# Performance work log

Hardware: AMD Instinct MI355X
Metric: run time of the kernel (lower is better)

Reference implementation:

```python
import jax, jax.numpy as jnp
import numpy as np

N_TOTAL = 524288  # total entity embeddings in flat ragged buffer
A = 262144        # number of actors
D = 256           # d_model
C = 32            # n_choice


def setup_inputs() -> dict:
    key = jax.random.key(0)
    k1, k2, k3, k4, k5 = jax.random.split(key, 5)
    x_data = jax.random.normal(k1, (N_TOTAL, D), dtype=jnp.float32)
    W = jax.random.normal(k2, (C, D), dtype=jnp.float32) * 0.01  # layer_init std=0.01
    b = jnp.zeros((C,), dtype=jnp.float32)
    actors = jax.random.randint(k3, (A,), 0, N_TOTAL, dtype=jnp.int64)
    mask = jax.random.randint(k4, (A, C), 0, 2, dtype=jnp.int32)
    mask = mask.at[:, 0].set(1)  # guarantee at least one valid choice per actor
    pa = jax.random.randint(k5, (A,), 0, C, dtype=jnp.int64)
    # prev_actions must be valid under the mask (as a real rollout would be)
    valid = jnp.take_along_axis(mask, pa[:, None], axis=1).squeeze(-1)
    prev_actions = jnp.where(valid != 0, pa, 0)
    return {"x_data": x_data, "W": W, "b": b, "actors": actors,
            "mask": mask, "prev_actions": prev_actions}


def reference(x_data, W, b, actors, mask, prev_actions):
    # gather actor embeddings: [A, D]
    actor_embeds = x_data[actors]
    # linear projection: [A, C]
    logits = jnp.einsum('ad,cd->ac', actor_embeds, W) + b
    # masked fill with -inf where mask == 0
    logits = jnp.where(mask == 0, -jnp.inf, logits)
    # Categorical: normalized logits = log_softmax
    logp = jax.nn.log_softmax(logits, axis=-1)
    p = jnp.exp(logp)
    action = prev_actions  # prev_actions provided -> no sampling
    logprob = jnp.take_along_axis(logp, action[:, None], axis=1).squeeze(-1)
    # entropy: -sum p*logp over valid entries (0*(-inf) -> 0)
    entropy = -jnp.sum(jnp.where(mask != 0, p * logp, 0.0), axis=-1)
    return action, logprob, entropy, logp
```

## Files before the change

### kernel.cpp

```cpp
#include <hip/hip_runtime.h>
#include <math.h>


constexpr int A_TOTAL = 262144;
constexpr int DMODEL  = 256;
constexpr int NCHOICE = 32;
constexpr int APB     = 64;
constexpr int PADC    = 36;

#define MASK_NEG 1.0e30f

#define DPP_SUM_STEP(x, ctrl)                                              \
    (x) += __int_as_float(__builtin_amdgcn_update_dpp(                     \
        0, __float_as_int(x), (ctrl), 0xf, 0xf, true))
#define DPP_MAX_STEP(x, ctrl)                                              \
    (x) = fmaxf((x), __int_as_float(__builtin_amdgcn_update_dpp(           \
        0, __float_as_int(x), (ctrl), 0xf, 0xf, true)))

#define DPP_REDUCE_DG(x)                                                   \
    do { DPP_SUM_STEP(x, 0xB1); DPP_SUM_STEP(x, 0x4E);                     \
         DPP_SUM_STEP(x, 0x128); DPP_SUM_STEP(x, 0x124); } while (0)
#define DPP_RED8_SUM(x)                                                    \
    do { DPP_SUM_STEP(x, 0xB1); DPP_SUM_STEP(x, 0x4E);                     \
         DPP_SUM_STEP(x, 0x141); } while (0)
#define DPP_RED8_MAX(x)                                                    \
    do { DPP_MAX_STEP(x, 0xB1); DPP_MAX_STEP(x, 0x4E);                     \
         DPP_MAX_STEP(x, 0x141); } while (0)

__global__ __launch_bounds__(256, 2)
void cat_action_head(const float* __restrict__ x_data,
                     const float* __restrict__ W,
                     const float* __restrict__ bvec,
                     const int*   __restrict__ actors,
                     const int*   __restrict__ mask,
                     const int*   __restrict__ prev_actions,
                     float* __restrict__ out)
{
    const int t  = threadIdx.x;
    const int wv = t >> 6;
    const int ln = t & 63;
    const int dg = ln & 15;
    const int cg = ln >> 4;

    float* out_action  = out;
    float* out_logprob = out + A_TOTAL;
    float* out_entropy = out + 2 * A_TOTAL;
    float* out_logp    = out + 3 * A_TOTAL;

    __shared__ float xs[4][2][8][DMODEL];
    __shared__ float part[APB][PADC];

    const int bbase = blockIdx.x * APB;
    const int wb    = bbase + wv * 16;

    const int q  = ln & 7;
    const int p0 = wv * 16 + (ln >> 3);
    const int p1 = p0 + 8;
    const int a0 = bbase + p0;
    const int a1 = bbase + p1;
    const int4   mv0 = *reinterpret_cast<const int4*>(&mask[(size_t)a0 * NCHOICE + q * 4]);
    const int4   mv1 = *reinterpret_cast<const int4*>(&mask[(size_t)a1 * NCHOICE + q * 4]);
    const float4 bq  = *reinterpret_cast<const float4*>(&bvec[q * 4]);
    const int    act0 = prev_actions[a0];
    const int    act1 = prev_actions[a1];

    int acts[16];
    {
        const int4 v0 = *reinterpret_cast<const int4*>(&actors[wb]);
        const int4 v1 = *reinterpret_cast<const int4*>(&actors[wb + 4]);
        const int4 v2 = *reinterpret_cast<const int4*>(&actors[wb + 8]);
        const int4 v3 = *reinterpret_cast<const int4*>(&actors[wb + 12]);
        acts[0]=v0.x; acts[1]=v0.y; acts[2]=v0.z; acts[3]=v0.w;
        acts[4]=v1.x; acts[5]=v1.y; acts[6]=v1.z; acts[7]=v1.w;
        acts[8]=v2.x; acts[9]=v2.y; acts[10]=v2.z; acts[11]=v2.w;
        acts[12]=v3.x; acts[13]=v3.y; acts[14]=v3.z; acts[15]=v3.w;
    }

#define STAGE(BUF, C)                                                       \
    do {                                                                    \
        _Pragma("unroll")                                                   \
        for (int j = 0; j < 8; ++j) {                                       \
            const float* src = x_data + (size_t)acts[(C) * 8 + j] * DMODEL  \
                             + ln * 4;                                      \
            __builtin_amdgcn_global_load_lds(                               \
                (const __attribute__((address_space(1))) void*)src,         \
                (__attribute__((address_space(3))) void*)&xs[wv][BUF][j][0],\
                16, 0, 0);                                                  \
        }                                                                   \
    } while (0)

    STAGE(0, 0);

    float4 Wf[8][4];
#pragma unroll
    for (int k = 0; k < 8; ++k) {
        const float* Wr = W + (size_t)(cg * 8 + k) * DMODEL + dg * 4;
#pragma unroll
        for (int j = 0; j < 4; ++j)
            Wf[k][j] = *reinterpret_cast<const float4*>(Wr + j * 64);
    }

    STAGE(1, 1);

#define LDR(DST, BUF, II)                                                   \
    do {                                                                    \
        const float* xrow_ = &xs[wv][BUF][II][dg * 4];                      \
        _Pragma("unroll")                                                   \
        for (int j = 0; j < 4; ++j)                                         \
            DST[j] = *reinterpret_cast<const float4*>(xrow_ + j * 64);      \
    } while (0)

#define COMPUTE(XV, C, II)                                                  \
    do {                                                                    \
        float acc[8] = {0.f,0.f,0.f,0.f,0.f,0.f,0.f,0.f};                   \
        _Pragma("unroll")                                                   \
        for (int j = 0; j < 4; ++j) {                                       \
            _Pragma("unroll")                                               \
            for (int k = 0; k < 8; ++k) {                                   \
                acc[k] = fmaf(XV[j].x, Wf[k][j].x, acc[k]);                 \
                acc[k] = fmaf(XV[j].y, Wf[k][j].y, acc[k]);                 \
                acc[k] = fmaf(XV[j].z, Wf[k][j].z, acc[k]);                 \
                acc[k] = fmaf(XV[j].w, Wf[k][j].w, acc[k]);                 \
            }                                                               \
        }                                                                   \
        _Pragma("unroll")                                                   \
        for (int k = 0; k < 8; ++k) DPP_REDUCE_DG(acc[k]);                  \
        if (dg == 0) {                                                      \
            const int p_ = wv * 16 + (C) * 8 + (II);                        \
            float4 v0_; v0_.x=acc[0]; v0_.y=acc[1]; v0_.z=acc[2]; v0_.w=acc[3]; \
            float4 v1_; v1_.x=acc[4]; v1_.y=acc[5]; v1_.z=acc[6]; v1_.w=acc[7]; \
            *reinterpret_cast<float4*>(&part[p_][cg * 8])     = v0_;        \
            *reinterpret_cast<float4*>(&part[p_][cg * 8 + 4]) = v1_;        \
        }                                                                   \
    } while (0)

#define GEMV_CHUNK(C)                                                       \
    do {                                                                    \
        float4 xva[4], xvb[4];                                              \
        LDR(xva, (C) & 1, 0);                                               \
        _Pragma("unroll")                                                   \
        for (int ii = 0; ii < 8; ii += 2) {                                 \
            if (ii + 1 < 8) LDR(xvb, (C) & 1, ii + 1);                      \
            COMPUTE(xva, C, ii);                                            \
            if (ii + 2 < 8) LDR(xva, (C) & 1, ii + 2);                      \
            COMPUTE(xvb, C, ii + 1);                                        \
        }                                                                   \
    } while (0)

    asm volatile("s_waitcnt vmcnt(8)" ::: "memory");
    GEMV_CHUNK(0);
    asm volatile("s_waitcnt vmcnt(0)" ::: "memory");
    GEMV_CHUNK(1);

#define EPILOGUE(PROW, AEP, MV, ACT)                                        \
    do {                                                                    \
        const float4 pv = *reinterpret_cast<const float4*>(&part[PROW][q * 4]); \
        const float lg0 = (MV).x ? pv.x + bq.x : -MASK_NEG;                 \
        const float lg1 = (MV).y ? pv.y + bq.y : -MASK_NEG;                 \
        const float lg2 = (MV).z ? pv.z + bq.z : -MASK_NEG;                 \
        const float lg3 = (MV).w ? pv.w + bq.w : -MASK_NEG;                 \
        float mx = fmaxf(fmaxf(lg0, lg1), fmaxf(lg2, lg3));                 \
        DPP_RED8_MAX(mx);                                                   \
        const float e0 = expf(lg0 - mx);                                    \
        const float e1 = expf(lg1 - mx);                                    \
        const float e2 = expf(lg2 - mx);                                    \
        const float e3 = expf(lg3 - mx);                                    \
        float se = (e0 + e1) + (e2 + e3);                                   \
        DPP_RED8_SUM(se);                                                   \
        const float lse = mx + logf(se);                                    \
        const float rse = 1.0f / se;                                        \
        const float lp0 = lg0 - lse;                                        \
        const float lp1 = lg1 - lse;                                        \
        const float lp2 = lg2 - lse;                                        \
        const float lp3 = lg3 - lse;                                        \
        float4 lpv; lpv.x=lp0; lpv.y=lp1; lpv.z=lp2; lpv.w=lp3;             \
        *reinterpret_cast<float4*>(                                         \
            &out_logp[(size_t)(AEP) * NCHOICE + q * 4]) = lpv;              \
        float ent = fmaf(e0, lp0, fmaf(e1, lp1, fmaf(e2, lp2, e3 * lp3)));  \
        DPP_RED8_SUM(ent);                                                  \
        float sel = ((ACT) == q * 4 + 0) ? lp0 : 0.0f;                      \
        sel = ((ACT) == q * 4 + 1) ? lp1 : sel;                             \
        sel = ((ACT) == q * 4 + 2) ? lp2 : sel;                             \
        sel = ((ACT) == q * 4 + 3) ? lp3 : sel;                             \
        DPP_RED8_SUM(sel);                                                  \
        if (q == 0) {                                                       \
            out_logprob[AEP] = sel;                                         \
            out_entropy[AEP] = -ent * rse;                                  \
            out_action[AEP]  = (float)(ACT);                                \
        }                                                                   \
    } while (0)

    EPILOGUE(p0, a0, mv0, act0);
    EPILOGUE(p1, a1, mv1, act1);

#undef EPILOGUE
#undef GEMV_CHUNK
#undef COMPUTE
#undef LDR
#undef STAGE
}

extern "C" void kernel_launch(void* const* d_in, const int* in_sizes, int n_in,
                              void* d_out, int out_size, void* d_ws, size_t ws_size,
                              hipStream_t stream)
{
    const float* x_data = (const float*)d_in[0];
    const float* W      = (const float*)d_in[1];
    const float* bvec   = (const float*)d_in[2];
    const int*   actors = (const int*)d_in[3];
    const int*   mask   = (const int*)d_in[4];
    const int*   prev   = (const int*)d_in[5];
    float*       o      = (float*)d_out;

    const int nblocks = A_TOTAL / APB;
    cat_action_head<<<nblocks, 256, 0, stream>>>(x_data, W, bvec, actors, mask,
                                                 prev, o);
}
```

Measured before the change: 94.75 us.

## Make each wave loop over 128 actors with double-buffered gathers

Each wave now processes 128 actors in 16 chunks of 8 instead of 16 actors, keeping W in registers across all chunks. This cuts the per-wave reloading of the 32 KB weight matrix and shrinks the grid from 4096 to 512 blocks. Gathers of the next chunk's embeddings go into LDS through global_load_lds while the current chunk is computed, and the actor indices, masks and previous actions are prefetched two chunks ahead. The pipeline depends on hand-tuned vmcnt wait counts, and a single wave of blocks gives less parallelism to hide latency with.

Result: slower. 97.29 us (+2.7%).

```diff
diff --git a/kernel.cpp b/kernel.cpp
--- a/kernel.cpp
+++ b/kernel.cpp
@@ -5,8 +5,9 @@
 constexpr int A_TOTAL = 262144;
 constexpr int DMODEL  = 256;
 constexpr int NCHOICE = 32;
-constexpr int APB     = 64;
 constexpr int PADC    = 36;
+constexpr int APW     = 128;
+constexpr int APB     = 512;
 
 #define MASK_NEG 1.0e30f
 
@@ -41,6 +42,8 @@
     const int ln = t & 63;
     const int dg = ln & 15;
     const int cg = ln >> 4;
+    const int q  = ln & 7;
+    const int ar = ln >> 3;
 
     float* out_action  = out;
     float* out_logprob = out + A_TOTAL;
@@ -48,117 +51,66 @@
     float* out_logp    = out + 3 * A_TOTAL;
 
     __shared__ float xs[4][2][8][DMODEL];
-    __shared__ float part[APB][PADC];
-
-    const int bbase = blockIdx.x * APB;
-    const int wb    = bbase + wv * 16;
-
-    const int q  = ln & 7;
-    const int p0 = wv * 16 + (ln >> 3);
-    const int p1 = p0 + 8;
-    const int a0 = bbase + p0;
-    const int a1 = bbase + p1;
-    const int4   mv0 = *reinterpret_cast<const int4*>(&mask[(size_t)a0 * NCHOICE + q * 4]);
-    const int4   mv1 = *reinterpret_cast<const int4*>(&mask[(size_t)a1 * NCHOICE + q * 4]);
-    const float4 bq  = *reinterpret_cast<const float4*>(&bvec[q * 4]);
-    const int    act0 = prev_actions[a0];
-    const int    act1 = prev_actions[a1];
-
-    int acts[16];
-    {
-        const int4 v0 = *reinterpret_cast<const int4*>(&actors[wb]);
-        const int4 v1 = *reinterpret_cast<const int4*>(&actors[wb + 4]);
-        const int4 v2 = *reinterpret_cast<const int4*>(&actors[wb + 8]);
-        const int4 v3 = *reinterpret_cast<const int4*>(&actors[wb + 12]);
-        acts[0]=v0.x; acts[1]=v0.y; acts[2]=v0.z; acts[3]=v0.w;
-        acts[4]=v1.x; acts[5]=v1.y; acts[6]=v1.z; acts[7]=v1.w;
-        acts[8]=v2.x; acts[9]=v2.y; acts[10]=v2.z; acts[11]=v2.w;
-        acts[12]=v3.x; acts[13]=v3.y; acts[14]=v3.z; acts[15]=v3.w;
-    }
-
-#define STAGE(BUF, C)                                                       \
-    do {                                                                    \
+    __shared__ float part[4][8][PADC];
+
+    const int wbase = (blockIdx.x * 4 + wv) * APW;
+
+#define STAGE(P, A0, A1)                                                    \
+    do {                                                                    \
+        const int av_[8] = {(A0).x,(A0).y,(A0).z,(A0).w,                    \
+                            (A1).x,(A1).y,(A1).z,(A1).w};                   \
         _Pragma("unroll")                                                   \
         for (int j = 0; j < 8; ++j) {                                       \
-            const float* src = x_data + (size_t)acts[(C) * 8 + j] * DMODEL  \
-                             + ln * 4;                                      \
+            const float* src_ = x_data + (size_t)av_[j] * DMODEL + ln * 4;  \
             __builtin_amdgcn_global_load_lds(                               \
-                (const __attribute__((address_space(1))) void*)src,         \
-                (__attribute__((address_space(3))) void*)&xs[wv][BUF][j][0],\
+                (const __attribute__((address_space(1))) void*)src_,        \
+                (__attribute__((address_space(3))) void*)&xs[wv][P][j][0],  \
                 16, 0, 0);                                                  \
         }                                                                   \
     } while (0)
 
-    STAGE(0, 0);
-
-    float4 Wf[8][4];
-#pragma unroll
-    for (int k = 0; k < 8; ++k) {
-        const float* Wr = W + (size_t)(cg * 8 + k) * DMODEL + dg * 4;
-#pragma unroll
-        for (int j = 0; j < 4; ++j)
-            Wf[k][j] = *reinterpret_cast<const float4*>(Wr + j * 64);
-    }
-
-    STAGE(1, 1);
-
-#define LDR(DST, BUF, II)                                                   \
-    do {                                                                    \
-        const float* xrow_ = &xs[wv][BUF][II][dg * 4];                      \
+#define GEMV(P)                                                             \
+    do {                                                                    \
         _Pragma("unroll")                                                   \
-        for (int j = 0; j < 4; ++j)                                         \
-            DST[j] = *reinterpret_cast<const float4*>(xrow_ + j * 64);      \
-    } while (0)
-
-#define COMPUTE(XV, C, II)                                                  \
-    do {                                                                    \
-        float acc[8] = {0.f,0.f,0.f,0.f,0.f,0.f,0.f,0.f};                   \
-        _Pragma("unroll")                                                   \
-        for (int j = 0; j < 4; ++j) {                                       \
+        for (int ii = 0; ii < 8; ++ii) {                                    \
+            const float* xrow_ = &xs[wv][P][ii][dg * 4];                    \
+            float4 xv_[4];                                                  \
             _Pragma("unroll")                                               \
-            for (int k = 0; k < 8; ++k) {                                   \
-                acc[k] = fmaf(XV[j].x, Wf[k][j].x, acc[k]);                 \
-                acc[k] = fmaf(XV[j].y, Wf[k][j].y, acc[k]);                 \
-                acc[k] = fmaf(XV[j].z, Wf[k][j].z, acc[k]);                 \
-                acc[k] = fmaf(XV[j].w, Wf[k][j].w, acc[k]);                 \
+            for (int j = 0; j < 4; ++j)                                     \
+                xv_[j] = *reinterpret_cast<const float4*>(xrow_ + j * 64);  \
+            float acc_[8] = {0.f,0.f,0.f,0.f,0.f,0.f,0.f,0.f};              \
+            _Pragma("unroll")                                               \
+            for (int j = 0; j < 4; ++j) {                                   \
+                _Pragma("unroll")                                           \
+                for (int k2 = 0; k2 < 8; ++k2) {                            \
+                    acc_[k2] = fmaf(xv_[j].x, Wf[k2][j].x, acc_[k2]);       \
+                    acc_[k2] = fmaf(xv_[j].y, Wf[k2][j].y, acc_[k2]);       \
+                    acc_[k2] = fmaf(xv_[j].z, Wf[k2][j].z, acc_[k2]);       \
+                    acc_[k2] = fmaf(xv_[j].w, Wf[k2][j].w, acc_[k2]);       \
+                }                                                           \
             }                                                               \
-        }                                                                   \
-        _Pragma("unroll")                                                   \
-        for (int k = 0; k < 8; ++k) DPP_REDUCE_DG(acc[k]);                  \
-        if (dg == 0) {                                                      \
-            const int p_ = wv * 16 + (C) * 8 + (II);                        \
-            float4 v0_; v0_.x=acc[0]; v0_.y=acc[1]; v0_.z=acc[2]; v0_.w=acc[3]; \
-            float4 v1_; v1_.x=acc[4]; v1_.y=acc[5]; v1_.z=acc[6]; v1_.w=acc[7]; \
-            *reinterpret_cast<float4*>(&part[p_][cg * 8])     = v0_;        \
-            *reinterpret_cast<float4*>(&part[p_][cg * 8 + 4]) = v1_;        \
-        }                                                                   \
-    } while (0)
-
-#define GEMV_CHUNK(C)                                                       \
-    do {                                                                    \
-        float4 xva[4], xvb[4];                                              \
-        LDR(xva, (C) & 1, 0);                                               \
-        _Pragma("unroll")                                                   \
-        for (int ii = 0; ii < 8; ii += 2) {                                 \
-            if (ii + 1 < 8) LDR(xvb, (C) & 1, ii + 1);                      \
-            COMPUTE(xva, C, ii);                                            \
-            if (ii + 2 < 8) LDR(xva, (C) & 1, ii + 2);                      \
-            COMPUTE(xvb, C, ii + 1);                                        \
-        }                                                                   \
-    } while (0)
-
-    asm volatile("s_waitcnt vmcnt(8)" ::: "memory");
-    GEMV_CHUNK(0);
-    asm volatile("s_waitcnt vmcnt(0)" ::: "memory");
-    GEMV_CHUNK(1);
-
-#define EPILOGUE(PROW, AEP, MV, ACT)                                        \
-    do {                                                                    \
-        const float4 pv = *reinterpret_cast<const float4*>(&part[PROW][q * 4]); \
-        const float lg0 = (MV).x ? pv.x + bq.x : -MASK_NEG;                 \
-        const float lg1 = (MV).y ? pv.y + bq.y : -MASK_NEG;                 \
-        const float lg2 = (MV).z ? pv.z + bq.z : -MASK_NEG;                 \
-        const float lg3 = (MV).w ? pv.w + bq.w : -MASK_NEG;                 \
+            _Pragma("unroll")                                               \
+            for (int k2 = 0; k2 < 8; ++k2) DPP_REDUCE_DG(acc_[k2]);         \
+            if (dg == 0) {                                                  \
+                float4 v0_; v0_.x=acc_[0]; v0_.y=acc_[1];                   \
+                            v0_.z=acc_[2]; v0_.w=acc_[3];                   \
+                float4 v1_; v1_.x=acc_[4]; v1_.y=acc_[5];                   \
+                            v1_.z=acc_[6]; v1_.w=acc_[7];                   \
+                *reinterpret_cast<float4*>(&part[wv][ii][cg * 8])     = v0_;\
+                *reinterpret_cast<float4*>(&part[wv][ii][cg * 8 + 4]) = v1_;\
+            }                                                               \
+        }                                                                   \
+    } while (0)
+
+#define EPI(K, MV, PV)                                                      \
+    do {                                                                    \
+        const int aep_ = wbase + (K) * 8 + ar;                              \
+        const float4 pv4_ =                                                 \
+            *reinterpret_cast<const float4*>(&part[wv][ar][q * 4]);         \
+        const float lg0 = (MV).x ? pv4_.x + bq.x : -MASK_NEG;               \
+        const float lg1 = (MV).y ? pv4_.y + bq.y : -MASK_NEG;               \
+        const float lg2 = (MV).z ? pv4_.z + bq.z : -MASK_NEG;               \
+        const float lg3 = (MV).w ? pv4_.w + bq.w : -MASK_NEG;               \
         float mx = fmaxf(fmaxf(lg0, lg1), fmaxf(lg2, lg3));                 \
         DPP_RED8_MAX(mx);                                                   \
         const float e0 = expf(lg0 - mx);                                    \
@@ -175,28 +127,80 @@
         const float lp3 = lg3 - lse;                                        \
         float4 lpv; lpv.x=lp0; lpv.y=lp1; lpv.z=lp2; lpv.w=lp3;             \
         *reinterpret_cast<float4*>(                                         \
-            &out_logp[(size_t)(AEP) * NCHOICE + q * 4]) = lpv;              \
+            &out_logp[(size_t)aep_ * NCHOICE + q * 4]) = lpv;               \
         float ent = fmaf(e0, lp0, fmaf(e1, lp1, fmaf(e2, lp2, e3 * lp3)));  \
         DPP_RED8_SUM(ent);                                                  \
-        float sel = ((ACT) == q * 4 + 0) ? lp0 : 0.0f;                      \
-        sel = ((ACT) == q * 4 + 1) ? lp1 : sel;                             \
-        sel = ((ACT) == q * 4 + 2) ? lp2 : sel;                             \
-        sel = ((ACT) == q * 4 + 3) ? lp3 : sel;                             \
+        float sel = ((PV) == q * 4 + 0) ? lp0 : 0.0f;                       \
+        sel = ((PV) == q * 4 + 1) ? lp1 : sel;                              \
+        sel = ((PV) == q * 4 + 2) ? lp2 : sel;                              \
+        sel = ((PV) == q * 4 + 3) ? lp3 : sel;                              \
         DPP_RED8_SUM(sel);                                                  \
         if (q == 0) {                                                       \
-            out_logprob[AEP] = sel;                                         \
-            out_entropy[AEP] = -ent * rse;                                  \
-            out_action[AEP]  = (float)(ACT);                                \
-        }                                                                   \
-    } while (0)
-
-    EPILOGUE(p0, a0, mv0, act0);
-    EPILOGUE(p1, a1, mv1, act1);
-
-#undef EPILOGUE
-#undef GEMV_CHUNK
-#undef COMPUTE
-#undef LDR
+            out_logprob[aep_] = sel;                                        \
+            out_entropy[aep_] = -ent * rse;                                 \
+            out_action[aep_]  = (float)(PV);                                \
+        }                                                                   \
+    } while (0)
+
+#define CHUNK(K, P, PN, AN0, AN1, AC0, AC1, MVV, PVV)                       \
+    do {                                                                    \
+        if ((K) == 0)                                                       \
+            asm volatile("s_waitcnt vmcnt(0)" ::: "memory");                \
+        else if ((K) == 15)                                                 \
+            asm volatile("s_waitcnt vmcnt(4)" ::: "memory");                \
+        else                                                                \
+            asm volatile("s_waitcnt vmcnt(6)" ::: "memory");                \
+        if ((K) < 15) STAGE(PN, AN0, AN1);                                  \
+        if ((K) < 14) {                                                     \
+            AC0 = *reinterpret_cast<const int4*>(                           \
+                      &actors[wbase + ((K) + 2) * 8]);                      \
+            AC1 = *reinterpret_cast<const int4*>(                           \
+                      &actors[wbase + ((K) + 2) * 8 + 4]);                  \
+        }                                                                   \
+        GEMV(P);                                                            \
+        EPI(K, MVV, PVV);                                                   \
+        if ((K) < 14) {                                                     \
+            MVV = *reinterpret_cast<const int4*>(                           \
+                &mask[(size_t)(wbase + ((K) + 2) * 8 + ar) * NCHOICE        \
+                      + q * 4]);                                            \
+            PVV = prev_actions[wbase + ((K) + 2) * 8 + ar];                 \
+        }                                                                   \
+    } while (0)
+
+    int4 aE0 = *reinterpret_cast<const int4*>(&actors[wbase + 0]);
+    int4 aE1 = *reinterpret_cast<const int4*>(&actors[wbase + 4]);
+    int4 aO0 = *reinterpret_cast<const int4*>(&actors[wbase + 8]);
+    int4 aO1 = *reinterpret_cast<const int4*>(&actors[wbase + 12]);
+    int4 mvE = *reinterpret_cast<const int4*>(
+                   &mask[(size_t)(wbase + ar) * NCHOICE + q * 4]);
+    int  pvE = prev_actions[wbase + ar];
+    int4 mvO = *reinterpret_cast<const int4*>(
+                   &mask[(size_t)(wbase + 8 + ar) * NCHOICE + q * 4]);
+    int  pvO = prev_actions[wbase + 8 + ar];
+    const float4 bq = *reinterpret_cast<const float4*>(&bvec[q * 4]);
+    asm volatile("s_waitcnt vmcnt(0)" ::: "memory");
+
+    float4 Wf[8][4];
+#pragma unroll
+    for (int k = 0; k < 8; ++k) {
+        const float* Wr = W + (size_t)(cg * 8 + k) * DMODEL + dg * 4;
+#pragma unroll
+        for (int j = 0; j < 4; ++j)
+            Wf[k][j] = *reinterpret_cast<const float4*>(Wr + j * 64);
+    }
+
+    STAGE(0, aE0, aE1);
+
+#pragma unroll 1
+    for (int o = 0; o < 8; ++o) {
+        const int k0 = 2 * o;
+        CHUNK(k0,     0, 1, aO0, aO1, aE0, aE1, mvE, pvE);
+        CHUNK(k0 + 1, 1, 0, aE0, aE1, aO0, aO1, mvO, pvO);
+    }
+
+#undef CHUNK
+#undef EPI
+#undef GEMV
 #undef STAGE
 }
 
```
